# Performance work log

Hardware: AMD Instinct MI355X
Metric: run time of the kernel (lower is better)

## Reference

```python
import jax, jax.numpy as jnp
import numpy as np

# LIF neuron constants (the CUDA kernel source is not shipped; these are the
# standard fused SNN semantics documented for this layer)
V_DECAY = 0.9       # membrane leak per step
V_THRESH = 1.0      # spike threshold
REFRAC_PERIOD = 5.0 # refractory timer reset value (in steps)

B_SZ, SEQ, HID, STATE = 8, 4096, 1024, 64


def setup_inputs() -> dict:
    key = jax.random.key(0)
    k1, k2, k3, k4, k5 = jax.random.split(key, 5)
    return {
        "input": jax.random.normal(k1, (B_SZ, SEQ, HID), dtype=jnp.float32),
        "ssm_A": jax.random.normal(k2, (STATE, STATE), dtype=jnp.float32) * 0.01,
        "ssm_B": jax.random.normal(k3, (STATE, 1), dtype=jnp.float32) * 0.1,
        "ssm_C": jax.random.normal(k4, (1, STATE), dtype=jnp.float32) * 0.1,
        "ssm_D": jax.random.normal(k5, (1, 1), dtype=jnp.float32) * 0.01,
    }


def reference(input, ssm_A, ssm_B, ssm_C, ssm_D):
    batch, seq_len, hidden = input.shape
    state = ssm_A.shape[0]

    # initial states (module.forward always starts from zeros)
    v0 = jnp.zeros((batch, hidden), dtype=jnp.float32)
    r0 = jnp.zeros((batch, hidden), dtype=jnp.float32)
    h0 = jnp.zeros((batch, state), dtype=jnp.float32)

    Bvec = ssm_B[:, 0]      # [state]
    Cvec = ssm_C[0, :]      # [state]
    Dsc = ssm_D[0, 0]       # scalar

    def step(carry, x_t):
        v, r, h = carry
        # --- SNN membrane + refractory update ---
        v = v * V_DECAY + x_t
        active = r <= 0.0
        spike = jnp.where(active & (v >= V_THRESH), 1.0, 0.0)  # [B,H]
        v = jnp.where(spike > 0.0, 0.0, v)
        r = jnp.where(spike > 0.0, REFRAC_PERIOD, jnp.maximum(r - 1.0, 0.0))
        # --- SSM recurrence, driven by pooled spike rate (scalar per batch) ---
        u = jnp.mean(spike, axis=-1)                 # [B]
        h = jnp.einsum('ns,bs->bn', ssm_A, h) + u[:, None] * Bvec  # [B,N]
        y = h @ Cvec + Dsc * u                       # [B]
        out_t = spike + y[:, None]                   # [B,H]
        return (v, r, h), out_t

    xs = jnp.swapaxes(input, 0, 1)                   # [S,B,H]
    _, ys = jax.lax.scan(step, (v0, r0, h0), xs)
    return jnp.swapaxes(ys, 0, 1)                    # [B,S,H]
```

## Files before the change

kernel.cpp:

```cpp
#include <hip/hip_runtime.h>
#include <cstdint>
#include <cstddef>

#define B_SZ   8
#define SEQ    4096
#define HID    1024
#define NCH    16
#define CHUNK  256
#define WARM   320
#define JTAP   16

#define YOFF   (131072)
#define WOFF   (262144)
#define SOFF   (262656)

__device__ __forceinline__ void snn_step(float& v, float& r, float xv, bool& s) {
  v = __fadd_rn(__fmul_rn(v, 0.9f), xv);
  s = (r <= 0.0f) && (v >= 1.0f);
  v = s ? 0.0f : v;
  r = s ? 5.0f : fmaxf(r - 1.0f, 0.0f);
}

__global__ __launch_bounds__(256) void snn_kernel(const float* __restrict__ x,
                                                  unsigned long long* __restrict__ spk) {
  const int hid  = blockIdx.x * 256 + threadIdx.x;
  const int b    = blockIdx.y;
  const int c    = blockIdx.z;
  const int lane = threadIdx.x & 63;
  const int wv   = hid >> 6;
  const int t0   = c * CHUNK;
  const int t1   = t0 + CHUNK;
  const int tw   = (t0 >= WARM) ? (t0 - WARM) : 0;
  const float* __restrict__ xp = x + (size_t)(b * SEQ) * HID + hid;
  unsigned long long* __restrict__ sp = spk + (size_t)(b * 16 + wv) * SEQ;

  float v = 0.0f, r = 0.0f;
  float xa[16], xb[16];

  #pragma unroll
  for (int k = 0; k < 16; ++k) xa[k] = xp[(size_t)(tw + k) * HID];

  for (int t = tw; t < t1; t += 32) {
    #pragma unroll
    for (int k = 0; k < 16; ++k) xb[k] = xp[(size_t)(t + 16 + k) * HID];

    if (t >= t0) {
      unsigned long long my = 0;
      #pragma unroll
      for (int k = 0; k < 16; ++k) {
        bool s; snn_step(v, r, xa[k], s);
        unsigned long long m = __ballot(s);
        if ((lane & 15) == k) my = m;
      }
      if (lane < 16) sp[t + lane] = my;
    } else {
      #pragma unroll
      for (int k = 0; k < 16; ++k) { bool s; snn_step(v, r, xa[k], s); }
    }

    if (t + 32 < t1) {
      #pragma unroll
      for (int k = 0; k < 16; ++k) xa[k] = xp[(size_t)(t + 32 + k) * HID];
    }

    if (t + 16 >= t0) {
      unsigned long long my = 0;
      #pragma unroll
      for (int k = 0; k < 16; ++k) {
        bool s; snn_step(v, r, xb[k], s);
        unsigned long long m = __ballot(s);
        if ((lane & 15) == k) my = m;
      }
      if (lane < 16) sp[t + 16 + lane] = my;
    } else {
      #pragma unroll
      for (int k = 0; k < 16; ++k) { bool s; snn_step(v, r, xb[k], s); }
    }
  }
}

__global__ void w_kernel(const float* __restrict__ A, const float* __restrict__ Bv,
                         const float* __restrict__ Cv, float* __restrict__ w) {
  const int lane = threadIdx.x;
  float arow[64];
  #pragma unroll 8
  for (int s = 0; s < 64; ++s) arow[s] = A[lane * 64 + s];
  float p = Bv[lane];
  float cv = Cv[lane];
  for (int m = 0; m < JTAP; ++m) {
    float t = cv * p;
    #pragma unroll
    for (int off = 32; off; off >>= 1) t += __shfl_xor(t, off);
    if (lane == 0) w[m] = t;
    float np = 0.0f;
    #pragma unroll 8
    for (int s = 0; s < 64; ++s) np = fmaf(arow[s], __shfl(p, s), np);
    p = np;
  }
}

__global__ __launch_bounds__(256) void y_kernel(const unsigned long long* __restrict__ spk,
                                                const float* __restrict__ w,
                                                const float* __restrict__ Dp,
                                                float* __restrict__ y) {
  __shared__ float su[CHUNK + JTAP];
  __shared__ float ws[JTAP];
  const int tid = threadIdx.x;
  const int b   = blockIdx.y;
  const int t0  = blockIdx.x * 256;
  const unsigned long long* __restrict__ sb = spk + (size_t)b * 16 * SEQ;

  if (tid < JTAP) ws[tid] = w[tid];
  {
    const int t = t0 + tid;
    int cc = 0;
    #pragma unroll
    for (int wv = 0; wv < 16; ++wv) cc += __popcll(sb[(size_t)wv * SEQ + t]);
    su[JTAP + tid] = cc * (1.0f / 1024.0f);
  }
  if (tid < JTAP) {
    const int t = t0 - JTAP + tid;
    int cc = 0;
    if (t >= 0) {
      #pragma unroll
      for (int wv = 0; wv < 16; ++wv) cc += __popcll(sb[(size_t)wv * SEQ + t]);
    }
    su[tid] = (t >= 0) ? cc * (1.0f / 1024.0f) : 0.0f;
  }
  __syncthreads();

  const float u = su[JTAP + tid];
  float acc = Dp[0] * u;
  #pragma unroll
  for (int m = 0; m < JTAP; ++m) acc = fmaf(ws[m], su[JTAP + tid - m], acc);
  y[b * SEQ + t0 + tid] = acc;
}

__global__ __launch_bounds__(256) void out_kernel(const unsigned long long* __restrict__ spk,
                                                  const float* __restrict__ y,
                                                  float4* __restrict__ out) {
  const int bt8  = blockIdx.x;
  const int b    = bt8 >> 9;
  const int tg   = bt8 & 511;
  const int lane = threadIdx.x;
  const int wv   = lane >> 4;
  const int sh   = (lane & 15) * 4;
  #pragma unroll
  for (int k = 0; k < 8; ++k) {
    const int t = tg * 8 + k;
    const unsigned long long m = spk[(size_t)(b * 16 + wv) * SEQ + t];
    const float yv = y[b * SEQ + t];
    float4 o;
    o.x = ((m >> (sh + 0)) & 1ull) ? 1.0f + yv : yv;
    o.y = ((m >> (sh + 1)) & 1ull) ? 1.0f + yv : yv;
    o.z = ((m >> (sh + 2)) & 1ull) ? 1.0f + yv : yv;
    o.w = ((m >> (sh + 3)) & 1ull) ? 1.0f + yv : yv;
    out[(size_t)(b * SEQ + t) * 256 + lane] = o;
  }
}

extern "C" void kernel_launch(void* const* d_in, const int* in_sizes, int n_in,
                              void* d_out, int out_size, void* d_ws, size_t ws_size,
                              hipStream_t stream) {
  const float* x  = (const float*)d_in[0];
  const float* A  = (const float*)d_in[1];
  const float* Bv = (const float*)d_in[2];
  const float* Cv = (const float*)d_in[3];
  const float* Dp = (const float*)d_in[4];
  float* out = (float*)d_out;

  char* ws = (char*)d_ws;
  float*              y   = (float*)(ws + YOFF);
  float*              w   = (float*)(ws + WOFF);
  unsigned long long* spk = (unsigned long long*)(ws + SOFF);

  w_kernel<<<1, 64, 0, stream>>>(A, Bv, Cv, w);

  dim3 g1(HID / 256, B_SZ, NCH);
  snn_kernel<<<g1, 256, 0, stream>>>(x, spk);

  dim3 g2(SEQ / 256, B_SZ);
  y_kernel<<<g2, 256, 0, stream>>>(spk, w, Dp, y);

  out_kernel<<<(B_SZ * SEQ) / 8, 256, 0, stream>>>(spk, y, (float4*)out);
}
```

Baseline: 283.3 us.

## Fuse tap, y and output kernels; widen SNN step batches to 32

Merges the filter-tap computation, the y convolution and the output expansion into one kernel per (time tile, batch). Each block recomputes the taps, stages spike masks in shared memory and writes the output tile, which removes two launches and the y round-trip through global memory. The SNN kernel now processes 32-step groups with 32-lane ballot packing, cutting loop overhead while increasing register pressure. Every block redundantly recomputes the 16 tap powers of A, adding serial work before the output stores.

```diff
diff --git a/kernel.cpp b/kernel.cpp
--- a/kernel.cpp
+++ b/kernel.cpp
@@ -9,16 +9,30 @@
 #define CHUNK  256
 #define WARM   320
 #define JTAP   16
-
-#define YOFF   (131072)
-#define WOFF   (262144)
-#define SOFF   (262656)
+#define TS     128
 
 __device__ __forceinline__ void snn_step(float& v, float& r, float xv, bool& s) {
   v = __fadd_rn(__fmul_rn(v, 0.9f), xv);
   s = (r <= 0.0f) && (v >= 1.0f);
   v = s ? 0.0f : v;
   r = s ? 5.0f : fmaxf(r - 1.0f, 0.0f);
+}
+
+__device__ __forceinline__ void proc32_emit(const float* xv, float& v, float& r, int lane,
+                                            unsigned long long* __restrict__ sp, int t) {
+  unsigned long long my = 0;
+  #pragma unroll
+  for (int k = 0; k < 32; ++k) {
+    bool s; snn_step(v, r, xv[k], s);
+    unsigned long long m = __ballot(s);
+    my = ((lane & 31) == k) ? m : my;
+  }
+  if (lane < 32) sp[t + lane] = my;
+}
+
+__device__ __forceinline__ void proc32_warm(const float* xv, float& v, float& r) {
+  #pragma unroll
+  for (int k = 0; k < 32; ++k) { bool s; snn_step(v, r, xv[k], s); }
 }
 
 __global__ __launch_bounds__(256) void snn_kernel(const float* __restrict__ x,
@@ -35,127 +49,106 @@
   unsigned long long* __restrict__ sp = spk + (size_t)(b * 16 + wv) * SEQ;
 
   float v = 0.0f, r = 0.0f;
-  float xa[16], xb[16];
+  float xa[32], xb[32];
 
   #pragma unroll
-  for (int k = 0; k < 16; ++k) xa[k] = xp[(size_t)(tw + k) * HID];
+  for (int k = 0; k < 32; ++k) xa[k] = xp[(size_t)(tw + k) * HID];
 
-  for (int t = tw; t < t1; t += 32) {
+  for (int t = tw; t < t1; t += 64) {
     #pragma unroll
-    for (int k = 0; k < 16; ++k) xb[k] = xp[(size_t)(t + 16 + k) * HID];
+    for (int k = 0; k < 32; ++k) xb[k] = xp[(size_t)(t + 32 + k) * HID];
 
-    if (t >= t0) {
-      unsigned long long my = 0;
+    if (t >= t0) proc32_emit(xa, v, r, lane, sp, t);
+    else         proc32_warm(xa, v, r);
+
+    if (t + 64 < t1) {
       #pragma unroll
-      for (int k = 0; k < 16; ++k) {
-        bool s; snn_step(v, r, xa[k], s);
-        unsigned long long m = __ballot(s);
-        if ((lane & 15) == k) my = m;
-      }
-      if (lane < 16) sp[t + lane] = my;
-    } else {
-      #pragma unroll
-      for (int k = 0; k < 16; ++k) { bool s; snn_step(v, r, xa[k], s); }
+      for (int k = 0; k < 32; ++k) xa[k] = xp[(size_t)(t + 64 + k) * HID];
     }
 
-    if (t + 32 < t1) {
-      #pragma unroll
-      for (int k = 0; k < 16; ++k) xa[k] = xp[(size_t)(t + 32 + k) * HID];
-    }
-
-    if (t + 16 >= t0) {
-      unsigned long long my = 0;
-      #pragma unroll
-      for (int k = 0; k < 16; ++k) {
-        bool s; snn_step(v, r, xb[k], s);
-        unsigned long long m = __ballot(s);
-        if ((lane & 15) == k) my = m;
-      }
-      if (lane < 16) sp[t + 16 + lane] = my;
-    } else {
-      #pragma unroll
-      for (int k = 0; k < 16; ++k) { bool s; snn_step(v, r, xb[k], s); }
-    }
+    if (t + 32 >= t0) proc32_emit(xb, v, r, lane, sp, t + 32);
+    else              proc32_warm(xb, v, r);
   }
 }
 
-__global__ void w_kernel(const float* __restrict__ A, const float* __restrict__ Bv,
-                         const float* __restrict__ Cv, float* __restrict__ w) {
-  const int lane = threadIdx.x;
-  float arow[64];
-  #pragma unroll 8
-  for (int s = 0; s < 64; ++s) arow[s] = A[lane * 64 + s];
-  float p = Bv[lane];
-  float cv = Cv[lane];
-  for (int m = 0; m < JTAP; ++m) {
-    float t = cv * p;
-    #pragma unroll
-    for (int off = 32; off; off >>= 1) t += __shfl_xor(t, off);
-    if (lane == 0) w[m] = t;
-    float np = 0.0f;
-    #pragma unroll 8
-    for (int s = 0; s < 64; ++s) np = fmaf(arow[s], __shfl(p, s), np);
-    p = np;
-  }
-}
+__global__ __launch_bounds__(256) void yout_kernel(const unsigned long long* __restrict__ spk,
+                                                   const float* __restrict__ A,
+                                                   const float* __restrict__ Bv,
+                                                   const float* __restrict__ Cv,
+                                                   const float* __restrict__ Dp,
+                                                   float4* __restrict__ out) {
+  __shared__ unsigned long long lm[16][TS + JTAP];
+  __shared__ float ws[JTAP];
+  __shared__ float su[TS + JTAP];
+  __shared__ float sy[TS];
 
-__global__ __launch_bounds__(256) void y_kernel(const unsigned long long* __restrict__ spk,
-                                                const float* __restrict__ w,
-                                                const float* __restrict__ Dp,
-                                                float* __restrict__ y) {
-  __shared__ float su[CHUNK + JTAP];
-  __shared__ float ws[JTAP];
   const int tid = threadIdx.x;
   const int b   = blockIdx.y;
-  const int t0  = blockIdx.x * 256;
+  const int t0  = blockIdx.x * TS;
   const unsigned long long* __restrict__ sb = spk + (size_t)b * 16 * SEQ;
 
-  if (tid < JTAP) ws[tid] = w[tid];
-  {
-    const int t = t0 + tid;
-    int cc = 0;
-    #pragma unroll
-    for (int wv = 0; wv < 16; ++wv) cc += __popcll(sb[(size_t)wv * SEQ + t]);
-    su[JTAP + tid] = cc * (1.0f / 1024.0f);
-  }
-  if (tid < JTAP) {
-    const int t = t0 - JTAP + tid;
-    int cc = 0;
-    if (t >= 0) {
+  if (tid < 64) {
+    const int lane = tid;
+    float arow[64];
+    #pragma unroll 8
+    for (int s2 = 0; s2 < 64; ++s2) arow[s2] = A[lane * 64 + s2];
+    float p = Bv[lane];
+    const float cv = Cv[lane];
+    for (int m = 0; m < JTAP; ++m) {
+      float t = cv * p;
       #pragma unroll
-      for (int wv = 0; wv < 16; ++wv) cc += __popcll(sb[(size_t)wv * SEQ + t]);
+      for (int off = 32; off; off >>= 1) t += __shfl_xor(t, off);
+      if (lane == 0) ws[m] = t;
+      float n0 = 0.f, n1 = 0.f, n2 = 0.f, n3 = 0.f;
+      #pragma unroll
+      for (int s2 = 0; s2 < 64; s2 += 4) {
+        n0 = fmaf(arow[s2 + 0], __shfl(p, s2 + 0), n0);
+        n1 = fmaf(arow[s2 + 1], __shfl(p, s2 + 1), n1);
+        n2 = fmaf(arow[s2 + 2], __shfl(p, s2 + 2), n2);
+        n3 = fmaf(arow[s2 + 3], __shfl(p, s2 + 3), n3);
+      }
+      p = (n0 + n1) + (n2 + n3);
     }
-    su[tid] = (t >= 0) ? cc * (1.0f / 1024.0f) : 0.0f;
+  } else {
+    const int i = tid - 64;
+    if (i < TS + JTAP) {
+      const int t = t0 - JTAP + i;
+      #pragma unroll
+      for (int wv = 0; wv < 16; ++wv)
+        lm[wv][i] = (t >= 0) ? sb[(size_t)wv * SEQ + t] : 0ull;
+    }
   }
   __syncthreads();
 
-  const float u = su[JTAP + tid];
-  float acc = Dp[0] * u;
-  #pragma unroll
-  for (int m = 0; m < JTAP; ++m) acc = fmaf(ws[m], su[JTAP + tid - m], acc);
-  y[b * SEQ + t0 + tid] = acc;
-}
+  if (tid < TS + JTAP) {
+    int cc = 0;
+    #pragma unroll
+    for (int wv = 0; wv < 16; ++wv) cc += __popcll(lm[wv][tid]);
+    su[tid] = cc * (1.0f / 1024.0f);
+  }
+  __syncthreads();
 
-__global__ __launch_bounds__(256) void out_kernel(const unsigned long long* __restrict__ spk,
-                                                  const float* __restrict__ y,
-                                                  float4* __restrict__ out) {
-  const int bt8  = blockIdx.x;
-  const int b    = bt8 >> 9;
-  const int tg   = bt8 & 511;
-  const int lane = threadIdx.x;
-  const int wv   = lane >> 4;
-  const int sh   = (lane & 15) * 4;
-  #pragma unroll
-  for (int k = 0; k < 8; ++k) {
-    const int t = tg * 8 + k;
-    const unsigned long long m = spk[(size_t)(b * 16 + wv) * SEQ + t];
-    const float yv = y[b * SEQ + t];
+  if (tid < TS) {
+    float acc = Dp[0] * su[JTAP + tid];
+    #pragma unroll
+    for (int m = 0; m < JTAP; ++m) acc = fmaf(ws[m], su[JTAP + tid - m], acc);
+    sy[tid] = acc;
+  }
+  __syncthreads();
+
+  const int wv = tid >> 4;
+  const int sh = (tid & 15) * 4;
+  float4* op = out + (size_t)(b * SEQ + t0) * 256 + tid;
+  #pragma unroll 4
+  for (int j = 0; j < TS; ++j) {
+    const unsigned long long m = lm[wv][JTAP + j];
+    const float yv = sy[j];
     float4 o;
     o.x = ((m >> (sh + 0)) & 1ull) ? 1.0f + yv : yv;
     o.y = ((m >> (sh + 1)) & 1ull) ? 1.0f + yv : yv;
     o.z = ((m >> (sh + 2)) & 1ull) ? 1.0f + yv : yv;
     o.w = ((m >> (sh + 3)) & 1ull) ? 1.0f + yv : yv;
-    out[(size_t)(b * SEQ + t) * 256 + lane] = o;
+    op[(size_t)j * 256] = o;
   }
 }
 
@@ -167,20 +160,12 @@
   const float* Bv = (const float*)d_in[2];
   const float* Cv = (const float*)d_in[3];
   const float* Dp = (const float*)d_in[4];
-  float* out = (float*)d_out;
 
-  char* ws = (char*)d_ws;
-  float*              y   = (float*)(ws + YOFF);
-  float*              w   = (float*)(ws + WOFF);
-  unsigned long long* spk = (unsigned long long*)(ws + SOFF);
-
-  w_kernel<<<1, 64, 0, stream>>>(A, Bv, Cv, w);
+  unsigned long long* spk = (unsigned long long*)d_ws;
 
   dim3 g1(HID / 256, B_SZ, NCH);
   snn_kernel<<<g1, 256, 0, stream>>>(x, spk);
 
-  dim3 g2(SEQ / 256, B_SZ);
-  y_kernel<<<g2, 256, 0, stream>>>(spk, w, Dp, y);
-
-  out_kernel<<<(B_SZ * SEQ) / 8, 256, 0, stream>>>(spk, y, (float4*)out);
+  dim3 g2(SEQ / TS, B_SZ);
+  yout_kernel<<<g2, 256, 0, stream>>>(spk, A, Bv, Cv, Dp, (float4*)d_out);
 }
```

Result: no change. 287.9 us (+1.6%).
